# Kernel tuning notes

Measured on AMD Instinct MI355X. Metric: run time of the kernel, lower is better.

The kernel has to match this reference:

```python
import jax, jax.numpy as jnp
import numpy as np

BN_EPS = 1e-5
K2 = 9  # 3x3 kernel


def _conv3x3(x, w, b):
    # x: [B,C,H,W], w: [O,C,3,3] -> [B,O,H,W], stride 1, pad 1
    out = jax.lax.conv_general_dilated(
        x, w, window_strides=(1, 1), padding=((1, 1), (1, 1)),
        dimension_numbers=("NCHW", "OIHW", "NCHW"))
    return out + b[None, :, None, None]


def setup_inputs() -> dict:
    key = jax.random.key(0)
    ks = jax.random.split(key, 8)
    B, C, H, W = 8, 256, 64, 64
    O = 256
    x = jax.random.normal(ks[0], (B, C, H, W), dtype=jnp.float32)
    # offset/mask conv: small init so sampled offsets stay near the base grid
    w_off = jax.random.normal(ks[1], (3 * K2, C, 3, 3), dtype=jnp.float32) * 0.01
    b_off = jnp.zeros((3 * K2,), dtype=jnp.float32)
    weight = jax.random.normal(ks[2], (O, C, 3, 3), dtype=jnp.float32) * 0.02
    bias = jnp.zeros((O,), dtype=jnp.float32)
    gamma = jnp.ones((O,), dtype=jnp.float32)
    beta = jnp.zeros((O,), dtype=jnp.float32)
    run_mean = jax.random.normal(ks[3], (O,), dtype=jnp.float32) * 0.1
    run_var = jax.random.uniform(ks[4], (O,), dtype=jnp.float32) + 0.5
    return {"x": x, "w_off": w_off, "b_off": b_off, "weight": weight,
            "bias": bias, "gamma": gamma, "beta": beta,
            "run_mean": run_mean, "run_var": run_var}


def _deform_sample(img, py, px):
    # img: [C,H,W]; py, px: [K2,H,W] sampling coordinates.
    # Bilinear sample with zero padding outside (DCNv2 semantics:
    # out-of-bounds corners contribute zero).
    C, H, W = img.shape
    y0 = jnp.floor(py)
    x0 = jnp.floor(px)
    wy1 = py - y0  # frac weights for the 'high' corner
    wx1 = px - x0

    def gather(yi, xi):
        valid = (yi >= 0) & (yi < H) & (xi >= 0) & (xi < W)
        yc = jnp.clip(yi, 0, H - 1).astype(jnp.int32)
        xc = jnp.clip(xi, 0, W - 1).astype(jnp.int32)
        return img[:, yc, xc] * valid.astype(img.dtype)[None]  # [C,K2,H,W]

    v00 = gather(y0, x0)
    v01 = gather(y0, x0 + 1)
    v10 = gather(y0 + 1, x0)
    v11 = gather(y0 + 1, x0 + 1)
    return (v00 * ((1 - wy1) * (1 - wx1))[None]
            + v01 * ((1 - wy1) * wx1)[None]
            + v10 * (wy1 * (1 - wx1))[None]
            + v11 * (wy1 * wx1)[None])  # [C,K2,H,W]


def reference(x, w_off, b_off, weight, bias, gamma, beta, run_mean, run_var):
    B, C, H, W = x.shape
    O = weight.shape[0]
    # 1) offset / mask branch (standard 3x3 conv)
    om = _conv3x3(x, w_off, b_off)  # [B, 27, H, W]
    off_y = om[:, :K2]
    off_x = om[:, K2:2 * K2]
    mask = jax.nn.sigmoid(om[:, 2 * K2:])  # modulation, [B,9,H,W]
    # 2) base sampling grid for 3x3, stride 1, pad 1, dilation 1
    ky = jnp.repeat(jnp.arange(3), 3).astype(x.dtype)  # [9]
    kx = jnp.tile(jnp.arange(3), 3).astype(x.dtype)    # [9]
    hs = jnp.arange(H, dtype=x.dtype)
    ws = jnp.arange(W, dtype=x.dtype)
    base_y = hs[None, :, None] - 1.0 + ky[:, None, None]  # [9,H,1]
    base_x = ws[None, None, :] - 1.0 + kx[:, None, None]  # [9,1,W]
    py = base_y[None] + off_y  # [B,9,H,W]
    px = base_x[None] + off_x
    # 3) modulated deformable im2col (bilinear gather) per batch
    cols = jax.vmap(_deform_sample)(x, py, px)  # [B,C,9,H,W]
    cols = cols * mask[:, None]                 # apply modulation mask
    # 4) GEMM over (C, K2) + bias
    w3 = weight.reshape(O, C, K2)
    out = jnp.einsum("ock,bckhw->bohw", w3, cols) + bias[None, :, None, None]
    # 5) BatchNorm (eval mode, running stats) + ReLU
    inv = gamma / jnp.sqrt(run_var + BN_EPS)
    out = out * inv[None, :, None, None] + (beta - run_mean * inv)[None, :, None, None]
    return jax.nn.relu(out)
```

## Files before the change

### kernel.cpp

```cpp
#include <hip/hip_runtime.h>
#include <math.h>

#define H 64
#define W 64
#define C 256
#define O 256
#define CK 2304
#define NB 8
#define HWSZ 4096

typedef __attribute__((ext_vector_type(8))) short short8;
typedef __attribute__((ext_vector_type(4))) float floatx4;
typedef __attribute__((ext_vector_type(4))) unsigned uintx4;

#define FSWZ(n) ((((n) & 3) << 1) | (((n) >> 2) & 1))

__device__ __forceinline__ unsigned short f2bf(float f) {
  unsigned u = __builtin_bit_cast(unsigned, f);
  unsigned r = (u + 0x7fffu + ((u >> 16) & 1u)) >> 16;
  return (unsigned short)r;
}
__device__ __forceinline__ float lo2f(unsigned u) {
  return __builtin_bit_cast(float, u << 16);
}
__device__ __forceinline__ float hi2f(unsigned u) {
  return __builtin_bit_cast(float, u & 0xffff0000u);
}
__device__ __forceinline__ unsigned pk2bf(float v0, float v1) {
  unsigned a = __builtin_bit_cast(unsigned, v0);
  unsigned b = __builtin_bit_cast(unsigned, v1);
  return ((a + 0x8000u) >> 16) | ((b + 0x8000u) & 0xffff0000u);
}

__global__ __launch_bounds__(256) void prep_all(
    const float* __restrict__ x, const float* __restrict__ weight,
    const float* __restrict__ w_off, const float* __restrict__ bias,
    const float* __restrict__ gamma, const float* __restrict__ beta,
    const float* __restrict__ run_mean, const float* __restrict__ run_var,
    unsigned short* __restrict__ xt, unsigned short* __restrict__ wb,
    unsigned short* __restrict__ wob, float* __restrict__ invsh) {
  __shared__ unsigned tile[64 * 65];
  int bid = blockIdx.x;
  int tid = threadIdx.x;

  if (bid < 1024) {
    int b = bid & 7;
    int t = bid >> 3;
    int y = t >> 1;
    int cg = t & 1;
    const float* xb = x + ((size_t)b * C + cg * 128) * HWSZ + y * W;
#pragma unroll
    for (int it = 0; it < 4; ++it) {
      int e = tid + 256 * it;
      int xx4 = e & 15;
      int cp = e >> 4;
      floatx4 f0 = *reinterpret_cast<const floatx4*>(
          xb + (size_t)(2 * cp) * HWSZ + xx4 * 4);
      floatx4 f1 = *reinterpret_cast<const floatx4*>(
          xb + (size_t)(2 * cp + 1) * HWSZ + xx4 * 4);
#pragma unroll
      for (int k = 0; k < 4; ++k)
        tile[cp * 65 + xx4 * 4 + k] = pk2bf(f0[k], f1[k]);
    }
    __syncthreads();
    unsigned short* xo = xt + ((size_t)(b * 64 + y) << 14) + cg * 128;
#pragma unroll
    for (int it = 0; it < 4; ++it) {
      int e = tid + 256 * it;
      int cq = e & 15;
      int xx = e >> 4;
      unsigned u0 = tile[(cq * 4 + 0) * 65 + xx];
      unsigned u1 = tile[(cq * 4 + 1) * 65 + xx];
      unsigned u2 = tile[(cq * 4 + 2) * 65 + xx];
      unsigned u3 = tile[(cq * 4 + 3) * 65 + xx];
      uint4 v = {u0, u1, u2, u3};
      *reinterpret_cast<uint4*>(xo + (xx << 8) + (cq << 3)) = v;
    }
  } else if (bid < 1312) {
    int d0 = ((bid - 1024) * 256 + tid) * 8;
    int lane = (d0 >> 3) & 63;
    int mt = (d0 >> 9) & 15;
    int ks = d0 >> 13;
    int o = mt * 16 + (lane & 15);
    int kn0 = ks * 32 + (lane >> 4) * 8;
    int tap = kn0 >> 8;
    int c0 = kn0 & 255;
    const float* wsrc = weight + o * CK + c0 * 9 + tap;
    unsigned pk[4];
#pragma unroll
    for (int p = 0; p < 4; ++p)
      pk[p] = pk2bf(wsrc[(2 * p) * 9], wsrc[(2 * p + 1) * 9]);
    uint4 v = {pk[0], pk[1], pk[2], pk[3]};
    *reinterpret_cast<uint4*>(wb + d0) = v;
  } else if (bid < 1348) {
    int d0 = ((bid - 1312) * 256 + tid) * 8;
    int lane = (d0 >> 3) & 63;
    int mt = (d0 >> 9) & 1;
    int ks = d0 >> 10;
    int o = mt * 16 + (lane & 15);
    int kn0 = ks * 32 + (lane >> 4) * 8;
    int tap = kn0 >> 8;
    int c0 = kn0 & 255;
    uint4 v;
    if (o < 27) {
      const float* wsrc = w_off + o * CK + c0 * 9 + tap;
      unsigned pk[4];
#pragma unroll
      for (int p = 0; p < 4; ++p)
        pk[p] = pk2bf(wsrc[(2 * p) * 9], wsrc[(2 * p + 1) * 9]);
      v = (uint4){pk[0], pk[1], pk[2], pk[3]};
    } else {
      v = (uint4){0, 0, 0, 0};
    }
    *reinterpret_cast<uint4*>(wob + d0) = v;
  } else {
    int o = tid;
    float inv = gamma[o] * rsqrtf(run_var[o] + 1e-5f);
    invsh[o] = inv;
    invsh[O + o] = beta[o] + (bias[o] - run_mean[o]) * inv;
  }
}

__global__ __launch_bounds__(512, 4) void deform_mfma_kernel(
    const unsigned short* __restrict__ xt, const unsigned short* __restrict__ wob,
    const float* __restrict__ b_off, const unsigned short* __restrict__ wb,
    const float* __restrict__ invsh, float* __restrict__ out) {
  __shared__ short cols[64 * 256];
  __shared__ float sm_om[27 * 64];
  __shared__ int sbase[576];
  __shared__ float s00[576], s01[576], s10[576], s11[576];

  int tid = threadIdx.x;
  int lane = tid & 63;
  int wvid = tid >> 6;
  int q = lane >> 4;
  int lm = lane & 15;
  int b = blockIdx.x;
  int h = blockIdx.y;
  const unsigned short* xtb = xt + ((size_t)b << 20);

  if (wvid < 4) {
    int mt = wvid & 1;
    int nh = wvid >> 1;
    floatx4 a0[2];
    a0[0] = (floatx4){0.f, 0.f, 0.f, 0.f};
    a0[1] = (floatx4){0.f, 0.f, 0.f, 0.f};
    int pxu[2];
    pxu[0] = (nh * 2 + 0) * 16 + lm;
    pxu[1] = (nh * 2 + 1) * 16 + lm;
    for (int tap = 0; tap < 9; ++tap) {
      int yy = h - 1 + tap / 3;
      bool vy = (yy >= 0) && (yy < H);
      const unsigned short* bp[2];
      bool vv[2];
#pragma unroll
      for (int u = 0; u < 2; ++u) {
        int xx = pxu[u] - 1 + tap % 3;
        vv[u] = vy && (xx >= 0) && (xx < W);
        bp[u] = xtb + ((((yy & 63) << 6) + (xx & 63)) << 8) + q * 8;
      }
#pragma unroll
      for (int s = 0; s < 8; ++s) {
        int ks = tap * 8 + s;
        short8 afrag = *reinterpret_cast<const short8*>(
            wob + (((ks * 2 + mt) * 64 + lane) << 3));
#pragma unroll
        for (int u = 0; u < 2; ++u) {
          short8 bfrag;
          if (vv[u])
            bfrag = *reinterpret_cast<const short8*>(bp[u] + s * 32);
          else
            bfrag = (short8){0, 0, 0, 0, 0, 0, 0, 0};
          a0[u] = __builtin_amdgcn_mfma_f32_16x16x32_bf16(afrag, bfrag, a0[u], 0, 0, 0);
        }
      }
    }
#pragma unroll
    for (int u = 0; u < 2; ++u)
#pragma unroll
      for (int r = 0; r < 4; ++r) {
        int o = mt * 16 + q * 4 + r;
        if (o < 27) sm_om[o * 64 + pxu[u]] = a0[u][r] + b_off[o];
      }
  }
  __syncthreads();

  for (int e = tid; e < 576; e += 512) {
    int n = e & 63;
    int k = e >> 6;
    float oy = sm_om[k * 64 + n];
    float ox = sm_om[(9 + k) * 64 + n];
    float mv = sm_om[(18 + k) * 64 + n];
    float m = 1.0f / (1.0f + __expf(-mv));
    float py = (float)(h - 1 + k / 3) + oy;
    float px = (float)(n - 1 + k % 3) + ox;
    float yf = floorf(py), xf = floorf(px);
    int y0 = (int)yf, x0 = (int)xf;
    float fy = py - yf, fx = px - xf;
    float r0, r1; int yl;
    if (y0 >= 0 && y0 <= H - 2)      { yl = y0;    r0 = 1.f - fy; r1 = fy;       }
    else if (y0 == -1)               { yl = 0;     r0 = fy;       r1 = 0.f;      }
    else if (y0 == H - 1)            { yl = H - 2; r0 = 0.f;      r1 = 1.f - fy; }
    else                             { yl = 0;     r0 = 0.f;      r1 = 0.f;      }
    float c0, c1; int xl;
    if (x0 >= 0 && x0 <= W - 2)      { xl = x0;    c0 = 1.f - fx; c1 = fx;       }
    else if (x0 == -1)               { xl = 0;     c0 = fx;       c1 = 0.f;      }
    else if (x0 == W - 1)            { xl = W - 2; c0 = 0.f;      c1 = 1.f - fx; }
    else                             { xl = 0;     c0 = 0.f;      c1 = 0.f;      }
    r0 *= m; r1 *= m;
    sbase[e] = ((yl << 6) + xl) << 8;
    s00[e] = r0 * c0; s01[e] = r0 * c1;
    s10[e] = r1 * c0; s11[e] = r1 * c1;
  }
  __syncthreads();

  floatx4 acc[2][4];
#pragma unroll
  for (int a = 0; a < 2; ++a)
#pragma unroll
    for (int u = 0; u < 4; ++u) acc[a][u] = (floatx4){0.f, 0.f, 0.f, 0.f};

  int sn = tid >> 3;
  int scb = tid & 7;

  for (int tap = 0; tap < 9; ++tap) {
    if (tap) __syncthreads();
    {
      int ei = tap * 64 + sn;
      int base = sbase[ei];
      float w00 = s00[ei], w01 = s01[ei], w10 = s10[ei], w11 = s11[ei];
      const unsigned short* p = xtb + base;
#pragma unroll
      for (int i = 0; i < 4; ++i) {
        int cbw = (i << 3) | scb;
        int co = cbw << 3;
        uintx4 u00 = *reinterpret_cast<const uintx4*>(p + co);
        uintx4 u01 = *reinterpret_cast<const uintx4*>(p + 256 + co);
        uintx4 u10 = *reinterpret_cast<const uintx4*>(p + 16384 + co);
        uintx4 u11 = *reinterpret_cast<const uintx4*>(p + 16640 + co);
        uintx4 res;
#pragma unroll
        for (int jd = 0; jd < 4; ++jd) {
          float v0 = fmaf(w00, lo2f(u00[jd]),
                     fmaf(w01, lo2f(u01[jd]),
                     fmaf(w10, lo2f(u10[jd]), w11 * lo2f(u11[jd]))));
          float v1 = fmaf(w00, hi2f(u00[jd]),
                     fmaf(w01, hi2f(u01[jd]),
                     fmaf(w10, hi2f(u10[jd]), w11 * hi2f(u11[jd]))));
          res[jd] = pk2bf(v0, v1);
        }
        int pos = (cbw ^ FSWZ(sn)) & 31;
        *reinterpret_cast<uintx4*>(&cols[(sn << 8) + (pos << 3)]) = res;
      }
    }
    __syncthreads();

#pragma unroll
    for (int s = 0; s < 8; ++s) {
      int ks = tap * 8 + s;
      short8 afrag[2];
#pragma unroll
      for (int a = 0; a < 2; ++a)
        afrag[a] = *reinterpret_cast<const short8*>(
            wb + (((ks * 16 + wvid * 2 + a) * 64 + lane) << 3));
      short8 bfrag[4];
#pragma unroll
      for (int u = 0; u < 4; ++u) {
        int nn = u * 16 + lm;
        int pos = ((s * 4 + q) ^ FSWZ(nn)) & 31;
        bfrag[u] = *reinterpret_cast<const short8*>(&cols[(nn << 8) + (pos << 3)]);
      }
#pragma unroll
      for (int a = 0; a < 2; ++a)
#pragma unroll
        for (int u = 0; u < 4; ++u)
          acc[a][u] = __builtin_amdgcn_mfma_f32_16x16x32_bf16(
              afrag[a], bfrag[u], acc[a][u], 0, 0, 0);
    }
  }

#pragma unroll
  for (int a = 0; a < 2; ++a) {
#pragma unroll
    for (int u = 0; u < 4; ++u) {
      int nn = u * 16 + lm;
#pragma unroll
      for (int r = 0; r < 4; ++r) {
        int o = (wvid * 2 + a) * 16 + q * 4 + r;
        float v = fmaf(acc[a][u][r], invsh[o], invsh[O + o]);
        out[((size_t)(b * O + o)) * HWSZ + h * W + nn] = fmaxf(v, 0.0f);
      }
    }
  }
}

extern "C" void kernel_launch(void* const* d_in, const int* in_sizes, int n_in,
                              void* d_out, int out_size, void* d_ws, size_t ws_size,
                              hipStream_t stream) {
  const float* x        = (const float*)d_in[0];
  const float* w_off    = (const float*)d_in[1];
  const float* b_off    = (const float*)d_in[2];
  const float* weight   = (const float*)d_in[3];
  const float* bias     = (const float*)d_in[4];
  const float* gamma    = (const float*)d_in[5];
  const float* beta     = (const float*)d_in[6];
  const float* run_mean = (const float*)d_in[7];
  const float* run_var  = (const float*)d_in[8];
  float* out = (float*)d_out;

  char* ws = (char*)d_ws;
  unsigned short* xt = (unsigned short*)ws;
  unsigned short* wbf = (unsigned short*)(ws + 16777216);
  unsigned short* wob = (unsigned short*)(ws + 17956864);
  float* invsh = (float*)(ws + 18104320);

  prep_all<<<1349, 256, 0, stream>>>(x, weight, w_off, bias, gamma, beta,
                                     run_mean, run_var, xt, wbf, wob, invsh);
  {
    dim3 grid(NB, H);
    deform_mfma_kernel<<<grid, 512, 0, stream>>>(xt, wob, b_off, wbf, invsh, out);
  }
}
```

Before: 191.5 us.

## Double-buffer deformable im2col tile and overlap sampling with MFMA via wave staggering

The cols LDS tile is double-buffered, so bilinear sampling for the next tap is written while MFMAs consume the current tap, with one barrier per tap instead of two. Odd and even waves run MFMA-then-sample versus sample-then-MFMA, and the MFMA phase raises wave priority with s_setprio, so memory and matrix work interleave across waves. The offset conv now spreads over all 8 waves with one accumulator each, and its output reuses the first cols buffer instead of separate LDS. The second buffer doubles cols LDS (about 64KB plus sample tables), which can lower occupancy below the 4-block launch bound target.

```diff
diff --git a/kernel.cpp b/kernel.cpp
--- a/kernel.cpp
+++ b/kernel.cpp
@@ -15,11 +15,6 @@
 
 #define FSWZ(n) ((((n) & 3) << 1) | (((n) >> 2) & 1))
 
-__device__ __forceinline__ unsigned short f2bf(float f) {
-  unsigned u = __builtin_bit_cast(unsigned, f);
-  unsigned r = (u + 0x7fffu + ((u >> 16) & 1u)) >> 16;
-  return (unsigned short)r;
-}
 __device__ __forceinline__ float lo2f(unsigned u) {
   return __builtin_bit_cast(float, u << 16);
 }
@@ -121,14 +116,77 @@
   }
 }
 
+__device__ __forceinline__ void sample_tap(
+    int tap, const unsigned short* __restrict__ xtb, short* __restrict__ colbuf,
+    const int* __restrict__ sbase, const float* __restrict__ s00,
+    const float* __restrict__ s01, const float* __restrict__ s10,
+    const float* __restrict__ s11, int sn, int scb) {
+  int ei = tap * 64 + sn;
+  int base = sbase[ei];
+  float w00 = s00[ei], w01 = s01[ei], w10 = s10[ei], w11 = s11[ei];
+  const unsigned short* p = xtb + base;
+#pragma unroll
+  for (int i = 0; i < 4; ++i) {
+    int cbw = (i << 3) | scb;
+    int co = cbw << 3;
+    uintx4 u00 = *reinterpret_cast<const uintx4*>(p + co);
+    uintx4 u01 = *reinterpret_cast<const uintx4*>(p + 256 + co);
+    uintx4 u10 = *reinterpret_cast<const uintx4*>(p + 16384 + co);
+    uintx4 u11 = *reinterpret_cast<const uintx4*>(p + 16640 + co);
+    uintx4 res;
+#pragma unroll
+    for (int jd = 0; jd < 4; ++jd) {
+      float v0 = fmaf(w00, lo2f(u00[jd]),
+                 fmaf(w01, lo2f(u01[jd]),
+                 fmaf(w10, lo2f(u10[jd]), w11 * lo2f(u11[jd]))));
+      float v1 = fmaf(w00, hi2f(u00[jd]),
+                 fmaf(w01, hi2f(u01[jd]),
+                 fmaf(w10, hi2f(u10[jd]), w11 * hi2f(u11[jd]))));
+      res[jd] = pk2bf(v0, v1);
+    }
+    int pos = (cbw ^ FSWZ(sn)) & 31;
+    *reinterpret_cast<uintx4*>(&colbuf[(sn << 8) + (pos << 3)]) = res;
+  }
+}
+
+__device__ __forceinline__ void mfma_tap(
+    int tap, const unsigned short* __restrict__ wb,
+    const short* __restrict__ colbuf, int wvid, int lane, int q, int lm,
+    floatx4 (&acc)[2][4]) {
+  __builtin_amdgcn_s_setprio(1);
+#pragma unroll
+  for (int s = 0; s < 8; ++s) {
+    int ks = tap * 8 + s;
+    short8 afrag[2];
+#pragma unroll
+    for (int a = 0; a < 2; ++a)
+      afrag[a] = *reinterpret_cast<const short8*>(
+          wb + (((ks * 16 + wvid * 2 + a) * 64 + lane) << 3));
+    short8 bfrag[4];
+#pragma unroll
+    for (int u = 0; u < 4; ++u) {
+      int nn = u * 16 + lm;
+      int pos = ((s * 4 + q) ^ FSWZ(nn)) & 31;
+      bfrag[u] = *reinterpret_cast<const short8*>(&colbuf[(nn << 8) + (pos << 3)]);
+    }
+#pragma unroll
+    for (int a = 0; a < 2; ++a)
+#pragma unroll
+      for (int u = 0; u < 4; ++u)
+        acc[a][u] = __builtin_amdgcn_mfma_f32_16x16x32_bf16(
+            afrag[a], bfrag[u], acc[a][u], 0, 0, 0);
+  }
+  __builtin_amdgcn_s_setprio(0);
+}
+
 __global__ __launch_bounds__(512, 4) void deform_mfma_kernel(
     const unsigned short* __restrict__ xt, const unsigned short* __restrict__ wob,
     const float* __restrict__ b_off, const unsigned short* __restrict__ wb,
     const float* __restrict__ invsh, float* __restrict__ out) {
-  __shared__ short cols[64 * 256];
-  __shared__ float sm_om[27 * 64];
+  __shared__ short cols[2][64 * 256];
   __shared__ int sbase[576];
   __shared__ float s00[576], s01[576], s10[576], s11[576];
+  float* sm_om = reinterpret_cast<float*>(&cols[0][0]);
 
   int tid = threadIdx.x;
   int lane = tid & 63;
@@ -139,49 +197,35 @@
   int h = blockIdx.y;
   const unsigned short* xtb = xt + ((size_t)b << 20);
 
-  if (wvid < 4) {
+  {
     int mt = wvid & 1;
-    int nh = wvid >> 1;
-    floatx4 a0[2];
-    a0[0] = (floatx4){0.f, 0.f, 0.f, 0.f};
-    a0[1] = (floatx4){0.f, 0.f, 0.f, 0.f};
-    int pxu[2];
-    pxu[0] = (nh * 2 + 0) * 16 + lm;
-    pxu[1] = (nh * 2 + 1) * 16 + lm;
+    int nq = wvid >> 1;
+    floatx4 a0 = (floatx4){0.f, 0.f, 0.f, 0.f};
+    int pxn = nq * 16 + lm;
     for (int tap = 0; tap < 9; ++tap) {
       int yy = h - 1 + tap / 3;
-      bool vy = (yy >= 0) && (yy < H);
-      const unsigned short* bp[2];
-      bool vv[2];
-#pragma unroll
-      for (int u = 0; u < 2; ++u) {
-        int xx = pxu[u] - 1 + tap % 3;
-        vv[u] = vy && (xx >= 0) && (xx < W);
-        bp[u] = xtb + ((((yy & 63) << 6) + (xx & 63)) << 8) + q * 8;
-      }
+      int xx = pxn - 1 + tap % 3;
+      bool vv = (yy >= 0) && (yy < H) && (xx >= 0) && (xx < W);
+      const unsigned short* bp =
+          xtb + ((((yy & 63) << 6) + (xx & 63)) << 8) + q * 8;
 #pragma unroll
       for (int s = 0; s < 8; ++s) {
         int ks = tap * 8 + s;
         short8 afrag = *reinterpret_cast<const short8*>(
             wob + (((ks * 2 + mt) * 64 + lane) << 3));
-#pragma unroll
-        for (int u = 0; u < 2; ++u) {
-          short8 bfrag;
-          if (vv[u])
-            bfrag = *reinterpret_cast<const short8*>(bp[u] + s * 32);
-          else
-            bfrag = (short8){0, 0, 0, 0, 0, 0, 0, 0};
-          a0[u] = __builtin_amdgcn_mfma_f32_16x16x32_bf16(afrag, bfrag, a0[u], 0, 0, 0);
-        }
+        short8 bfrag;
+        if (vv)
+          bfrag = *reinterpret_cast<const short8*>(bp + s * 32);
+        else
+          bfrag = (short8){0, 0, 0, 0, 0, 0, 0, 0};
+        a0 = __builtin_amdgcn_mfma_f32_16x16x32_bf16(afrag, bfrag, a0, 0, 0, 0);
       }
     }
 #pragma unroll
-    for (int u = 0; u < 2; ++u)
-#pragma unroll
-      for (int r = 0; r < 4; ++r) {
-        int o = mt * 16 + q * 4 + r;
-        if (o < 27) sm_om[o * 64 + pxu[u]] = a0[u][r] + b_off[o];
-      }
+    for (int r = 0; r < 4; ++r) {
+      int o = mt * 16 + q * 4 + r;
+      if (o < 27) sm_om[o * 64 + pxn] = a0[r] + b_off[o];
+    }
   }
   __syncthreads();
 
@@ -223,60 +267,22 @@
   int sn = tid >> 3;
   int scb = tid & 7;
 
+  sample_tap(0, xtb, cols[0], sbase, s00, s01, s10, s11, sn, scb);
+  __syncthreads();
+
   for (int tap = 0; tap < 9; ++tap) {
-    if (tap) __syncthreads();
-    {
-      int ei = tap * 64 + sn;
-      int base = sbase[ei];
-      float w00 = s00[ei], w01 = s01[ei], w10 = s10[ei], w11 = s11[ei];
-      const unsigned short* p = xtb + base;
-#pragma unroll
-      for (int i = 0; i < 4; ++i) {
-        int cbw = (i << 3) | scb;
-        int co = cbw << 3;
-        uintx4 u00 = *reinterpret_cast<const uintx4*>(p + co);
-        uintx4 u01 = *reinterpret_cast<const uintx4*>(p + 256 + co);
-        uintx4 u10 = *reinterpret_cast<const uintx4*>(p + 16384 + co);
-        uintx4 u11 = *reinterpret_cast<const uintx4*>(p + 16640 + co);
-        uintx4 res;
-#pragma unroll
-        for (int jd = 0; jd < 4; ++jd) {
-          float v0 = fmaf(w00, lo2f(u00[jd]),
-                     fmaf(w01, lo2f(u01[jd]),
-                     fmaf(w10, lo2f(u10[jd]), w11 * lo2f(u11[jd]))));
-          float v1 = fmaf(w00, hi2f(u00[jd]),
-                     fmaf(w01, hi2f(u01[jd]),
-                     fmaf(w10, hi2f(u10[jd]), w11 * hi2f(u11[jd]))));
-          res[jd] = pk2bf(v0, v1);
-        }
-        int pos = (cbw ^ FSWZ(sn)) & 31;
-        *reinterpret_cast<uintx4*>(&cols[(sn << 8) + (pos << 3)]) = res;
-      }
+    short* cur = cols[tap & 1];
+    short* nxt = cols[(tap + 1) & 1];
+    if (wvid & 1) {
+      mfma_tap(tap, wb, cur, wvid, lane, q, lm, acc);
+      if (tap < 8)
+        sample_tap(tap + 1, xtb, nxt, sbase, s00, s01, s10, s11, sn, scb);
+    } else {
+      if (tap < 8)
+        sample_tap(tap + 1, xtb, nxt, sbase, s00, s01, s10, s11, sn, scb);
+      mfma_tap(tap, wb, cur, wvid, lane, q, lm, acc);
     }
     __syncthreads();
-
-#pragma unroll
-    for (int s = 0; s < 8; ++s) {
-      int ks = tap * 8 + s;
-      short8 afrag[2];
-#pragma unroll
-      for (int a = 0; a < 2; ++a)
-        afrag[a] = *reinterpret_cast<const short8*>(
-            wb + (((ks * 16 + wvid * 2 + a) * 64 + lane) << 3));
-      short8 bfrag[4];
-#pragma unroll
-      for (int u = 0; u < 4; ++u) {
-        int nn = u * 16 + lm;
-        int pos = ((s * 4 + q) ^ FSWZ(nn)) & 31;
-        bfrag[u] = *reinterpret_cast<const short8*>(&cols[(nn << 8) + (pos << 3)]);
-      }
-#pragma unroll
-      for (int a = 0; a < 2; ++a)
-#pragma unroll
-        for (int u = 0; u < 4; ++u)
-          acc[a][u] = __builtin_amdgcn_mfma_f32_16x16x32_bf16(
-              afrag[a], bfrag[u], acc[a][u], 0, 0, 0);
-    }
   }
 
 #pragma unroll
```

Result: no change. 195.0 us (+1.8%).

## Split each row into two 32-pixel halves to double grid size

Applied to the files above, without the earlier changes.

The main kernel now handles half a row (32 pixels) per block, with the grid extended along z. This doubles the block count from 512 to 1024 so work spreads more evenly across CUs, and it shrinks LDS use by aliasing the offset buffer onto the cols buffer. In exchange, each block reloads the full weight matrix for half the output, so weight traffic per output doubles and MFMA work per sync shrinks. It also raises wave priority around the MFMA section with s_setprio.

```diff
diff --git a/kernel.cpp b/kernel.cpp
--- a/kernel.cpp
+++ b/kernel.cpp
@@ -8,6 +8,7 @@
 #define CK 2304
 #define NB 8
 #define HWSZ 4096
+#define PX 32
 
 typedef __attribute__((ext_vector_type(8))) short short8;
 typedef __attribute__((ext_vector_type(4))) float floatx4;
@@ -15,11 +16,6 @@
 
 #define FSWZ(n) ((((n) & 3) << 1) | (((n) >> 2) & 1))
 
-__device__ __forceinline__ unsigned short f2bf(float f) {
-  unsigned u = __builtin_bit_cast(unsigned, f);
-  unsigned r = (u + 0x7fffu + ((u >> 16) & 1u)) >> 16;
-  return (unsigned short)r;
-}
 __device__ __forceinline__ float lo2f(unsigned u) {
   return __builtin_bit_cast(float, u << 16);
 }
@@ -125,10 +121,10 @@
     const unsigned short* __restrict__ xt, const unsigned short* __restrict__ wob,
     const float* __restrict__ b_off, const unsigned short* __restrict__ wb,
     const float* __restrict__ invsh, float* __restrict__ out) {
-  __shared__ short cols[64 * 256];
-  __shared__ float sm_om[27 * 64];
-  __shared__ int sbase[576];
-  __shared__ float s00[576], s01[576], s10[576], s11[576];
+  __shared__ short cols[PX * 256];
+  __shared__ int sbase[9 * PX];
+  __shared__ float s00[9 * PX], s01[9 * PX], s10[9 * PX], s11[9 * PX];
+  float* sm_om = reinterpret_cast<float*>(&cols[0]);
 
   int tid = threadIdx.x;
   int lane = tid & 63;
@@ -137,63 +133,51 @@
   int lm = lane & 15;
   int b = blockIdx.x;
   int h = blockIdx.y;
+  int half = blockIdx.z;
   const unsigned short* xtb = xt + ((size_t)b << 20);
 
   if (wvid < 4) {
     int mt = wvid & 1;
     int nh = wvid >> 1;
-    floatx4 a0[2];
-    a0[0] = (floatx4){0.f, 0.f, 0.f, 0.f};
-    a0[1] = (floatx4){0.f, 0.f, 0.f, 0.f};
-    int pxu[2];
-    pxu[0] = (nh * 2 + 0) * 16 + lm;
-    pxu[1] = (nh * 2 + 1) * 16 + lm;
+    floatx4 a0 = (floatx4){0.f, 0.f, 0.f, 0.f};
+    int pxn = nh * 16 + lm;
+    int pxg = half * PX + pxn;
     for (int tap = 0; tap < 9; ++tap) {
       int yy = h - 1 + tap / 3;
-      bool vy = (yy >= 0) && (yy < H);
-      const unsigned short* bp[2];
-      bool vv[2];
-#pragma unroll
-      for (int u = 0; u < 2; ++u) {
-        int xx = pxu[u] - 1 + tap % 3;
-        vv[u] = vy && (xx >= 0) && (xx < W);
-        bp[u] = xtb + ((((yy & 63) << 6) + (xx & 63)) << 8) + q * 8;
-      }
+      int xx = pxg - 1 + tap % 3;
+      bool vv = (yy >= 0) && (yy < H) && (xx >= 0) && (xx < W);
+      const unsigned short* bp =
+          xtb + ((((yy & 63) << 6) + (xx & 63)) << 8) + q * 8;
 #pragma unroll
       for (int s = 0; s < 8; ++s) {
         int ks = tap * 8 + s;
         short8 afrag = *reinterpret_cast<const short8*>(
             wob + (((ks * 2 + mt) * 64 + lane) << 3));
-#pragma unroll
-        for (int u = 0; u < 2; ++u) {
-          short8 bfrag;
-          if (vv[u])
-            bfrag = *reinterpret_cast<const short8*>(bp[u] + s * 32);
-          else
-            bfrag = (short8){0, 0, 0, 0, 0, 0, 0, 0};
-          a0[u] = __builtin_amdgcn_mfma_f32_16x16x32_bf16(afrag, bfrag, a0[u], 0, 0, 0);
-        }
+        short8 bfrag;
+        if (vv)
+          bfrag = *reinterpret_cast<const short8*>(bp + s * 32);
+        else
+          bfrag = (short8){0, 0, 0, 0, 0, 0, 0, 0};
+        a0 = __builtin_amdgcn_mfma_f32_16x16x32_bf16(afrag, bfrag, a0, 0, 0, 0);
       }
     }
 #pragma unroll
-    for (int u = 0; u < 2; ++u)
-#pragma unroll
-      for (int r = 0; r < 4; ++r) {
-        int o = mt * 16 + q * 4 + r;
-        if (o < 27) sm_om[o * 64 + pxu[u]] = a0[u][r] + b_off[o];
-      }
+    for (int r = 0; r < 4; ++r) {
+      int o = mt * 16 + q * 4 + r;
+      if (o < 27) sm_om[o * PX + pxn] = a0[r] + b_off[o];
+    }
   }
   __syncthreads();
 
-  for (int e = tid; e < 576; e += 512) {
-    int n = e & 63;
-    int k = e >> 6;
-    float oy = sm_om[k * 64 + n];
-    float ox = sm_om[(9 + k) * 64 + n];
-    float mv = sm_om[(18 + k) * 64 + n];
+  if (tid < 9 * PX) {
+    int n = tid & (PX - 1);
+    int k = tid >> 5;
+    float oy = sm_om[k * PX + n];
+    float ox = sm_om[(9 + k) * PX + n];
+    float mv = sm_om[(18 + k) * PX + n];
     float m = 1.0f / (1.0f + __expf(-mv));
     float py = (float)(h - 1 + k / 3) + oy;
-    float px = (float)(n - 1 + k % 3) + ox;
+    float px = (float)(half * PX + n - 1 + k % 3) + ox;
     float yf = floorf(py), xf = floorf(px);
     int y0 = (int)yf, x0 = (int)xf;
     float fy = py - yf, fx = px - xf;
@@ -208,31 +192,31 @@
     else if (x0 == W - 1)            { xl = W - 2; c0 = 0.f;      c1 = 1.f - fx; }
     else                             { xl = 0;     c0 = 0.f;      c1 = 0.f;      }
     r0 *= m; r1 *= m;
-    sbase[e] = ((yl << 6) + xl) << 8;
-    s00[e] = r0 * c0; s01[e] = r0 * c1;
-    s10[e] = r1 * c0; s11[e] = r1 * c1;
+    sbase[tid] = ((yl << 6) + xl) << 8;
+    s00[tid] = r0 * c0; s01[tid] = r0 * c1;
+    s10[tid] = r1 * c0; s11[tid] = r1 * c1;
   }
   __syncthreads();
 
-  floatx4 acc[2][4];
+  floatx4 acc[2][2];
 #pragma unroll
   for (int a = 0; a < 2; ++a)
 #pragma unroll
-    for (int u = 0; u < 4; ++u) acc[a][u] = (floatx4){0.f, 0.f, 0.f, 0.f};
-
-  int sn = tid >> 3;
-  int scb = tid & 7;
+    for (int u = 0; u < 2; ++u) acc[a][u] = (floatx4){0.f, 0.f, 0.f, 0.f};
+
+  int sn = tid >> 4;
+  int scb = tid & 15;
 
   for (int tap = 0; tap < 9; ++tap) {
     if (tap) __syncthreads();
     {
-      int ei = tap * 64 + sn;
+      int ei = tap * PX + sn;
       int base = sbase[ei];
       float w00 = s00[ei], w01 = s01[ei], w10 = s10[ei], w11 = s11[ei];
       const unsigned short* p = xtb + base;
 #pragma unroll
-      for (int i = 0; i < 4; ++i) {
-        int cbw = (i << 3) | scb;
+      for (int i = 0; i < 2; ++i) {
+        int cbw = (i << 4) | scb;
         int co = cbw << 3;
         uintx4 u00 = *reinterpret_cast<const uintx4*>(p + co);
         uintx4 u01 = *reinterpret_cast<const uintx4*>(p + 256 + co);
@@ -255,6 +239,7 @@
     }
     __syncthreads();
 
+    __builtin_amdgcn_s_setprio(1);
 #pragma unroll
     for (int s = 0; s < 8; ++s) {
       int ks = tap * 8 + s;
@@ -263,9 +248,9 @@
       for (int a = 0; a < 2; ++a)
         afrag[a] = *reinterpret_cast<const short8*>(
             wb + (((ks * 16 + wvid * 2 + a) * 64 + lane) << 3));
-      short8 bfrag[4];
-#pragma unroll
-      for (int u = 0; u < 4; ++u) {
+      short8 bfrag[2];
+#pragma unroll
+      for (int u = 0; u < 2; ++u) {
         int nn = u * 16 + lm;
         int pos = ((s * 4 + q) ^ FSWZ(nn)) & 31;
         bfrag[u] = *reinterpret_cast<const short8*>(&cols[(nn << 8) + (pos << 3)]);
@@ -273,22 +258,24 @@
 #pragma unroll
       for (int a = 0; a < 2; ++a)
 #pragma unroll
-        for (int u = 0; u < 4; ++u)
+        for (int u = 0; u < 2; ++u)
           acc[a][u] = __builtin_amdgcn_mfma_f32_16x16x32_bf16(
               afrag[a], bfrag[u], acc[a][u], 0, 0, 0);
     }
+    __builtin_amdgcn_s_setprio(0);
   }
 
 #pragma unroll
   for (int a = 0; a < 2; ++a) {
 #pragma unroll
-    for (int u = 0; u < 4; ++u) {
+    for (int u = 0; u < 2; ++u) {
       int nn = u * 16 + lm;
 #pragma unroll
       for (int r = 0; r < 4; ++r) {
         int o = (wvid * 2 + a) * 16 + q * 4 + r;
         float v = fmaf(acc[a][u][r], invsh[o], invsh[O + o]);
-        out[((size_t)(b * O + o)) * HWSZ + h * W + nn] = fmaxf(v, 0.0f);
+        out[((size_t)(b * O + o)) * HWSZ + h * W + half * PX + nn] =
+            fmaxf(v, 0.0f);
       }
     }
   }
@@ -317,7 +304,7 @@
   prep_all<<<1349, 256, 0, stream>>>(x, weight, w_off, bias, gamma, beta,
                                      run_mean, run_var, xt, wbf, wob, invsh);
   {
-    dim3 grid(NB, H);
+    dim3 grid(NB, H, 2);
     deform_mfma_kernel<<<grid, 512, 0, stream>>>(xt, wob, b_off, wbf, invsh, out);
   }
 }
```

New measurement: 211.0 us. +10.1%, slower.
